# Performance work log

Hardware: AMD Instinct MI355X
Metric: run time of the kernel (lower is better)

## Reference

```python
import math
import jax, jax.numpy as jnp
import numpy as np

B_SZ = 32768   # batch (reflections)
S = 4          # mc_samples
D_IN = 256     # encoder dim
LAT = 8        # latent dim
NBINS = 300    # resolution x angle bins
K = 1323       # profile pixels
R = 4          # CP rank


def setup_inputs() -> dict:
    key = jax.random.key(0)
    ks = jax.random.split(key, 8)
    x = jax.random.normal(ks[0], (B_SZ, D_IN), jnp.float32)
    group_labels = jax.random.randint(ks[1], (B_SZ,), 0, NBINS)
    eps = jax.random.normal(ks[2], (S, B_SZ, LAT), jnp.float32)  # reparam noise
    A = jax.random.normal(ks[3], (NBINS, R), jnp.float32) * 0.01
    B = jax.random.normal(ks[4], (K, R), jnp.float32) * 0.01
    C = jax.random.normal(ks[5], (LAT, R), jnp.float32) * 0.01
    b = jnp.zeros((NBINS, K), jnp.float32)
    # nn.Linear default init (kaiming-uniform approx via small normal is fine for a numeric baseline)
    bound = 1.0 / math.sqrt(D_IN)
    mu_w = jax.random.uniform(ks[6], (LAT, D_IN), jnp.float32, -bound, bound)
    mu_b = jax.random.uniform(ks[7], (LAT,), jnp.float32, -bound, bound)
    std_w = jnp.zeros((LAT, D_IN), jnp.float32)  # nn.init.zeros_
    std_b = jnp.full((LAT,), math.log(math.exp(0.5) - 1.0), jnp.float32)  # softplus^-1(0.5)
    return dict(x=x, eps=eps, A=A, B=B, C=C, b=b, mu_w=mu_w, mu_b=mu_b,
                std_w=std_w, std_b=std_b, group_labels=group_labels)


def reference(x, eps, A, B, C, b, mu_w, mu_b, std_w, std_b, group_labels):
    mu_h = x @ mu_w.T + mu_b                      # (B, d)
    std_h = jax.nn.softplus(x @ std_w.T + std_b)  # (B, d)
    h = mu_h + std_h * eps                        # rsample: (S, B, d)

    A_n = A[group_labels]                         # (B, R)  per-bin gather
    b_n = b[group_labels]                         # (B, K)  per-bin gather

    z = h @ C                                     # (S, B, R)
    logits = (A_n * z) @ B.T + b_n                # (S, B, K)
    zp = jax.nn.softmax(logits, axis=-1)

    z_mean = mu_h @ C                             # (B, R)
    mean_logits = (A_n * z_mean) @ B.T + b_n      # (B, K)
    mean_profile = jax.nn.softmax(mean_logits, axis=-1)
    return zp, mean_profile, mu_h, std_h
```

## Files before the change

kernel.cpp:

```cpp
#include <hip/hip_runtime.h>

#define B_SZ  32768
#define S_MC  4
#define D_IN  256
#define LAT   8
#define NBINS 300
#define KDIM  1323
#define RNK   4

typedef float f32x4 __attribute__((ext_vector_type(4)));

constexpr int TPB   = 256;
constexpr int BPB   = 4;
constexpr int NPASS = S_MC + 1;
constexpr int NF4   = 330;
constexpr int ITER1 = NF4 - TPB;


__global__ __launch_bounds__(TPB) void cp_profile_kernel(
    const float* __restrict__ x,
    const float* __restrict__ eps,
    const float* __restrict__ A,
    const float* __restrict__ Bm,
    const float* __restrict__ C,
    const float* __restrict__ bias,
    const float* __restrict__ mu_w,
    const float* __restrict__ mu_b,
    const float* __restrict__ std_w,
    const float* __restrict__ std_b,
    const int*   __restrict__ glab,
    float* __restrict__ out)
{
    __shared__ float muh_s[LAT];
    __shared__ float stdh_s[LAT];
    __shared__ float w_s[NPASS][RNK];
    __shared__ float redmax_s[4][NPASS];
    __shared__ float redsum_s[4][NPASS];

    const int tid  = threadIdx.x;
    const int lane = tid & 63;
    const int wid  = tid >> 6;
    const f32x4* B4 = reinterpret_cast<const f32x4*>(Bm);

    for (int bb = 0; bb < BPB; ++bb) {
        const int b = blockIdx.x * BPB + bb;
        const int g = glab[b];
        const int p = b & 3;

        const f32x4* x4 = reinterpret_cast<const f32x4*>(x + (size_t)b * D_IN);
        const f32x4 xv = x4[lane];
        float dotv[4];
        #pragma unroll
        for (int dd = 0; dd < 4; ++dd) {
            const int d = wid * 4 + dd;
            const f32x4* W4 = reinterpret_cast<const f32x4*>(
                (d < LAT) ? (mu_w + d * D_IN) : (std_w + (d - LAT) * D_IN));
            const f32x4 wv = W4[lane];
            float a = xv.x * wv.x + xv.y * wv.y + xv.z * wv.z + xv.w * wv.w;
            #pragma unroll
            for (int off = 32; off > 0; off >>= 1)
                a += __shfl_xor(a, off, 64);
            dotv[dd] = a;
        }
        if (lane == 0) {
            #pragma unroll
            for (int dd = 0; dd < 4; ++dd) {
                const int d = wid * 4 + dd;
                if (d < LAT) {
                    muh_s[d] = dotv[dd] + mu_b[d];
                } else {
                    const float y = dotv[dd] + std_b[d - LAT];
                    stdh_s[d - LAT] = fmaxf(y, 0.f) + log1pf(expf(-fabsf(y)));
                }
            }
        }
        __syncthreads();

        if (tid < 20) {
            const int s = tid >> 2, r = tid & 3;
            const float* ep = eps + ((size_t)(s < S_MC ? s : 0) * B_SZ + b) * LAT;
            float z = 0.f;
            #pragma unroll
            for (int j = 0; j < LAT; ++j) {
                float h = muh_s[j];
                if (s < S_MC) h += stdh_s[j] * ep[j];
                z += h * C[j * RNK + r];
            }
            w_s[s][r] = A[g * RNK + r] * z;
        }
        const size_t base_small = (size_t)NPASS * B_SZ * KDIM;
        if (tid >= 32 && tid < 40)
            out[base_small + (size_t)b * LAT + (tid - 32)] = muh_s[tid - 32];
        if (tid >= 40 && tid < 48)
            out[base_small + (size_t)B_SZ * LAT + (size_t)b * LAT + (tid - 40)] = stdh_s[tid - 40];
        __syncthreads();

        float wr[NPASS][RNK];
        #pragma unroll
        for (int s = 0; s < NPASS; ++s)
            #pragma unroll
            for (int r = 0; r < RNK; ++r)
                wr[s][r] = w_s[s][r];

        const int  k0 = p + 4 * tid;
        const bool v1 = (tid < ITER1);
        const int  k1 = p + 4 * (TPB + tid);
        const int  e  = tid - 100;
        const bool vht = (e >= 0 && e < 3);
        const int  kht = vht ? ((e < p) ? e : (1320 + e)) : 0;

        const float* biasg = bias + (size_t)g * KDIM;
        f32x4 br0[4], br1[4];
        float bv0[4], bv1[4];
        #pragma unroll
        for (int q = 0; q < 4; ++q) {
            br0[q] = B4[k0 + q];
            bv0[q] = biasg[k0 + q];
            if (v1) { br1[q] = B4[k1 + q]; bv1[q] = biasg[k1 + q]; }
            else    { br1[q] = (f32x4)(0.f); bv1[q] = -INFINITY; }
        }
        f32x4 brht = (f32x4)(0.f);
        float bvht = -INFINITY;
        if (vht) { brht = B4[kht]; bvht = biasg[kht]; }

        auto LG = [&](const f32x4& r4, float bi, int s) -> float {
            return fmaf(wr[s][0], r4.x,
                   fmaf(wr[s][1], r4.y,
                   fmaf(wr[s][2], r4.z, wr[s][3] * r4.w))) + bi;
        };

        float lmax[NPASS];
        #pragma unroll
        for (int s = 0; s < NPASS; ++s) {
            float m0 = -INFINITY;
            #pragma unroll
            for (int q = 0; q < 4; ++q) {
                m0 = fmaxf(m0, LG(br0[q], bv0[q], s));
                m0 = fmaxf(m0, LG(br1[q], bv1[q], s));
            }
            lmax[s] = fmaxf(m0, LG(brht, bvht, s));
        }
        #pragma unroll
        for (int s = 0; s < NPASS; ++s)
            #pragma unroll
            for (int off = 32; off > 0; off >>= 1)
                lmax[s] = fmaxf(lmax[s], __shfl_xor(lmax[s], off, 64));
        if (lane == 0) {
            #pragma unroll
            for (int s = 0; s < NPASS; ++s) redmax_s[wid][s] = lmax[s];
        }
        __syncthreads();

        float m[NPASS];
        #pragma unroll
        for (int s = 0; s < NPASS; ++s)
            m[s] = fmaxf(fmaxf(redmax_s[0][s], redmax_s[1][s]),
                         fmaxf(redmax_s[2][s], redmax_s[3][s]));

        float lsum[NPASS];
        #pragma unroll
        for (int s = 0; s < NPASS; ++s) {
            float a = 0.f;
            #pragma unroll
            for (int q = 0; q < 4; ++q) {
                a += __expf(LG(br0[q], bv0[q], s) - m[s]);
                a += __expf(LG(br1[q], bv1[q], s) - m[s]);
            }
            lsum[s] = a + __expf(LG(brht, bvht, s) - m[s]);
        }
        #pragma unroll
        for (int s = 0; s < NPASS; ++s)
            #pragma unroll
            for (int off = 32; off > 0; off >>= 1)
                lsum[s] += __shfl_xor(lsum[s], off, 64);
        if (lane == 0) {
            #pragma unroll
            for (int s = 0; s < NPASS; ++s) redsum_s[wid][s] = lsum[s];
        }
        __syncthreads();

        float inv[NPASS];
        #pragma unroll
        for (int s = 0; s < NPASS; ++s)
            inv[s] = 1.f / (redsum_s[0][s] + redsum_s[1][s] +
                            redsum_s[2][s] + redsum_s[3][s]);

        #pragma unroll
        for (int s = 0; s < NPASS; ++s) {
            const size_t ob = (s < S_MC)
                ? ((size_t)((size_t)s * B_SZ + b) * KDIM)
                : ((size_t)S_MC * B_SZ * KDIM + (size_t)b * KDIM);
            f32x4 o0;
            o0.x = __expf(LG(br0[0], bv0[0], s) - m[s]) * inv[s];
            o0.y = __expf(LG(br0[1], bv0[1], s) - m[s]) * inv[s];
            o0.z = __expf(LG(br0[2], bv0[2], s) - m[s]) * inv[s];
            o0.w = __expf(LG(br0[3], bv0[3], s) - m[s]) * inv[s];
            __builtin_nontemporal_store(
                o0, reinterpret_cast<f32x4*>(out + ob + k0));
            if (v1) {
                f32x4 o1;
                o1.x = __expf(LG(br1[0], bv1[0], s) - m[s]) * inv[s];
                o1.y = __expf(LG(br1[1], bv1[1], s) - m[s]) * inv[s];
                o1.z = __expf(LG(br1[2], bv1[2], s) - m[s]) * inv[s];
                o1.w = __expf(LG(br1[3], bv1[3], s) - m[s]) * inv[s];
                __builtin_nontemporal_store(
                    o1, reinterpret_cast<f32x4*>(out + ob + k1));
            }
            if (vht) {
                const float v = __expf(LG(brht, bvht, s) - m[s]) * inv[s];
                __builtin_nontemporal_store(v, out + ob + kht);
            }
        }
    }
}

extern "C" void kernel_launch(void* const* d_in, const int* in_sizes, int n_in,
                              void* d_out, int out_size, void* d_ws, size_t ws_size,
                              hipStream_t stream) {
    const float* x     = (const float*)d_in[0];
    const float* eps   = (const float*)d_in[1];
    const float* A     = (const float*)d_in[2];
    const float* Bm    = (const float*)d_in[3];
    const float* C     = (const float*)d_in[4];
    const float* bias  = (const float*)d_in[5];
    const float* mu_w  = (const float*)d_in[6];
    const float* mu_b  = (const float*)d_in[7];
    const float* std_w = (const float*)d_in[8];
    const float* std_b = (const float*)d_in[9];
    const int*   glab  = (const int*)d_in[10];
    float* out = (float*)d_out;

    cp_profile_kernel<<<B_SZ / BPB, TPB, 0, stream>>>(
        x, eps, A, Bm, C, bias, mu_w, mu_b, std_w, std_b, glab, out);
}
```

Before: 1.109 ms.

## Use one wavefront per reflection with scalar strided stores and wave-only reductions

Restructures the kernel so each 64-thread block handles a single batch row, with every thread covering about 21 strided profile pixels. The cross-wave LDS reductions and their barriers go away, since the softmax max and sum reductions now stay inside one wavefront via shuffles. In exchange, the 16-byte vectorized output stores become scalar 4-byte stores, the grid grows to 32768 small blocks, and B rows are reloaded in each of the three passes. The output write bandwidth, which likely dominates, may suffer from the narrower stores.

```diff
diff --git a/kernel.cpp b/kernel.cpp
--- a/kernel.cpp
+++ b/kernel.cpp
@@ -10,14 +10,12 @@
 
 typedef float f32x4 __attribute__((ext_vector_type(4)));
 
-constexpr int TPB   = 256;
-constexpr int BPB   = 4;
+constexpr int TPB   = 64;
 constexpr int NPASS = S_MC + 1;
-constexpr int NF4   = 330;
-constexpr int ITER1 = NF4 - TPB;
+constexpr int KPT   = (KDIM + TPB - 1) / TPB;
 
 
-__global__ __launch_bounds__(TPB) void cp_profile_kernel(
+__global__ __launch_bounds__(TPB, 4) void cp_profile_kernel(
     const float* __restrict__ x,
     const float* __restrict__ eps,
     const float* __restrict__ A,
@@ -34,181 +32,132 @@
     __shared__ float muh_s[LAT];
     __shared__ float stdh_s[LAT];
     __shared__ float w_s[NPASS][RNK];
-    __shared__ float redmax_s[4][NPASS];
-    __shared__ float redsum_s[4][NPASS];
 
-    const int tid  = threadIdx.x;
-    const int lane = tid & 63;
-    const int wid  = tid >> 6;
+    const int t = threadIdx.x;
+    const int b = blockIdx.x;
+    const int g = glab[b];
+
+    {
+        const int d = t >> 2, c = t & 3;
+        const f32x4* x4 = reinterpret_cast<const f32x4*>(x + (size_t)b * D_IN);
+        const f32x4* W4 = reinterpret_cast<const f32x4*>(
+            (d < LAT) ? (mu_w + d * D_IN) : (std_w + (d - LAT) * D_IN));
+        float a = 0.f;
+        #pragma unroll
+        for (int i = 0; i < 16; ++i) {
+            const f32x4 xv = x4[c * 16 + i];
+            const f32x4 wv = W4[c * 16 + i];
+            a += xv.x * wv.x + xv.y * wv.y + xv.z * wv.z + xv.w * wv.w;
+        }
+        a += __shfl_xor(a, 1, 64);
+        a += __shfl_xor(a, 2, 64);
+        if (c == 0) {
+            if (d < LAT) {
+                muh_s[d] = a + mu_b[d];
+            } else {
+                const float y = a + std_b[d - LAT];
+                stdh_s[d - LAT] = fmaxf(y, 0.f) + log1pf(expf(-fabsf(y)));
+            }
+        }
+    }
+    __syncthreads();
+
+    if (t < 20) {
+        const int s = t >> 2, r = t & 3;
+        const float* ep = eps + ((size_t)(s < S_MC ? s : 0) * B_SZ + b) * LAT;
+        float z = 0.f;
+        #pragma unroll
+        for (int j = 0; j < LAT; ++j) {
+            float h = muh_s[j];
+            if (s < S_MC) h += stdh_s[j] * ep[j];
+            z += h * C[j * RNK + r];
+        }
+        w_s[s][r] = A[g * RNK + r] * z;
+    }
+    const size_t base_small = (size_t)NPASS * B_SZ * KDIM;
+    if (t >= 32 && t < 40)
+        out[base_small + (size_t)b * LAT + (t - 32)] = muh_s[t - 32];
+    if (t >= 40 && t < 48)
+        out[base_small + (size_t)B_SZ * LAT + (size_t)b * LAT + (t - 40)] = stdh_s[t - 40];
+    __syncthreads();
+
+    float wr[NPASS][RNK];
+    #pragma unroll
+    for (int s = 0; s < NPASS; ++s)
+        #pragma unroll
+        for (int r = 0; r < RNK; ++r)
+            wr[s][r] = w_s[s][r];
+
+    const float* biasg = bias + (size_t)g * KDIM;
+    float bn[KPT];
+    #pragma unroll
+    for (int j = 0; j < KPT; ++j) {
+        const int k = t + TPB * j;
+        bn[j] = (k < KDIM) ? biasg[k] : 0.f;
+    }
+
     const f32x4* B4 = reinterpret_cast<const f32x4*>(Bm);
 
-    for (int bb = 0; bb < BPB; ++bb) {
-        const int b = blockIdx.x * BPB + bb;
-        const int g = glab[b];
-        const int p = b & 3;
+    auto LG = [&](const f32x4& r4, float bi, int s) -> float {
+        return fmaf(wr[s][0], r4.x,
+               fmaf(wr[s][1], r4.y,
+               fmaf(wr[s][2], r4.z, wr[s][3] * r4.w))) + bi;
+    };
 
-        const f32x4* x4 = reinterpret_cast<const f32x4*>(x + (size_t)b * D_IN);
-        const f32x4 xv = x4[lane];
-        float dotv[4];
+    float lmax[NPASS];
+    #pragma unroll
+    for (int s = 0; s < NPASS; ++s) lmax[s] = -INFINITY;
+    #pragma unroll
+    for (int j = 0; j < KPT; ++j) {
+        const int k = t + TPB * j;
+        if (k < KDIM) {
+            const f32x4 bv = B4[k];
+            #pragma unroll
+            for (int s = 0; s < NPASS; ++s)
+                lmax[s] = fmaxf(lmax[s], LG(bv, bn[j], s));
+        }
+    }
+    #pragma unroll
+    for (int s = 0; s < NPASS; ++s)
         #pragma unroll
-        for (int dd = 0; dd < 4; ++dd) {
-            const int d = wid * 4 + dd;
-            const f32x4* W4 = reinterpret_cast<const f32x4*>(
-                (d < LAT) ? (mu_w + d * D_IN) : (std_w + (d - LAT) * D_IN));
-            const f32x4 wv = W4[lane];
-            float a = xv.x * wv.x + xv.y * wv.y + xv.z * wv.z + xv.w * wv.w;
+        for (int off = 32; off > 0; off >>= 1)
+            lmax[s] = fmaxf(lmax[s], __shfl_xor(lmax[s], off, 64));
+
+    float lsum[NPASS];
+    #pragma unroll
+    for (int s = 0; s < NPASS; ++s) lsum[s] = 0.f;
+    #pragma unroll
+    for (int j = 0; j < KPT; ++j) {
+        const int k = t + TPB * j;
+        if (k < KDIM) {
+            const f32x4 bv = B4[k];
             #pragma unroll
-            for (int off = 32; off > 0; off >>= 1)
-                a += __shfl_xor(a, off, 64);
-            dotv[dd] = a;
+            for (int s = 0; s < NPASS; ++s)
+                lsum[s] += __expf(LG(bv, bn[j], s) - lmax[s]);
         }
-        if (lane == 0) {
+    }
+    #pragma unroll
+    for (int s = 0; s < NPASS; ++s)
+        #pragma unroll
+        for (int off = 32; off > 0; off >>= 1)
+            lsum[s] += __shfl_xor(lsum[s], off, 64);
+
+    float inv[NPASS];
+    #pragma unroll
+    for (int s = 0; s < NPASS; ++s) inv[s] = 1.f / lsum[s];
+
+    #pragma unroll
+    for (int j = 0; j < KPT; ++j) {
+        const int k = t + TPB * j;
+        if (k < KDIM) {
+            const f32x4 bv = B4[k];
             #pragma unroll
-            for (int dd = 0; dd < 4; ++dd) {
-                const int d = wid * 4 + dd;
-                if (d < LAT) {
-                    muh_s[d] = dotv[dd] + mu_b[d];
-                } else {
-                    const float y = dotv[dd] + std_b[d - LAT];
-                    stdh_s[d - LAT] = fmaxf(y, 0.f) + log1pf(expf(-fabsf(y)));
-                }
-            }
-        }
-        __syncthreads();
-
-        if (tid < 20) {
-            const int s = tid >> 2, r = tid & 3;
-            const float* ep = eps + ((size_t)(s < S_MC ? s : 0) * B_SZ + b) * LAT;
-            float z = 0.f;
-            #pragma unroll
-            for (int j = 0; j < LAT; ++j) {
-                float h = muh_s[j];
-                if (s < S_MC) h += stdh_s[j] * ep[j];
-                z += h * C[j * RNK + r];
-            }
-            w_s[s][r] = A[g * RNK + r] * z;
-        }
-        const size_t base_small = (size_t)NPASS * B_SZ * KDIM;
-        if (tid >= 32 && tid < 40)
-            out[base_small + (size_t)b * LAT + (tid - 32)] = muh_s[tid - 32];
-        if (tid >= 40 && tid < 48)
-            out[base_small + (size_t)B_SZ * LAT + (size_t)b * LAT + (tid - 40)] = stdh_s[tid - 40];
-        __syncthreads();
-
-        float wr[NPASS][RNK];
-        #pragma unroll
-        for (int s = 0; s < NPASS; ++s)
-            #pragma unroll
-            for (int r = 0; r < RNK; ++r)
-                wr[s][r] = w_s[s][r];
-
-        const int  k0 = p + 4 * tid;
-        const bool v1 = (tid < ITER1);
-        const int  k1 = p + 4 * (TPB + tid);
-        const int  e  = tid - 100;
-        const bool vht = (e >= 0 && e < 3);
-        const int  kht = vht ? ((e < p) ? e : (1320 + e)) : 0;
-
-        const float* biasg = bias + (size_t)g * KDIM;
-        f32x4 br0[4], br1[4];
-        float bv0[4], bv1[4];
-        #pragma unroll
-        for (int q = 0; q < 4; ++q) {
-            br0[q] = B4[k0 + q];
-            bv0[q] = biasg[k0 + q];
-            if (v1) { br1[q] = B4[k1 + q]; bv1[q] = biasg[k1 + q]; }
-            else    { br1[q] = (f32x4)(0.f); bv1[q] = -INFINITY; }
-        }
-        f32x4 brht = (f32x4)(0.f);
-        float bvht = -INFINITY;
-        if (vht) { brht = B4[kht]; bvht = biasg[kht]; }
-
-        auto LG = [&](const f32x4& r4, float bi, int s) -> float {
-            return fmaf(wr[s][0], r4.x,
-                   fmaf(wr[s][1], r4.y,
-                   fmaf(wr[s][2], r4.z, wr[s][3] * r4.w))) + bi;
-        };
-
-        float lmax[NPASS];
-        #pragma unroll
-        for (int s = 0; s < NPASS; ++s) {
-            float m0 = -INFINITY;
-            #pragma unroll
-            for (int q = 0; q < 4; ++q) {
-                m0 = fmaxf(m0, LG(br0[q], bv0[q], s));
-                m0 = fmaxf(m0, LG(br1[q], bv1[q], s));
-            }
-            lmax[s] = fmaxf(m0, LG(brht, bvht, s));
-        }
-        #pragma unroll
-        for (int s = 0; s < NPASS; ++s)
-            #pragma unroll
-            for (int off = 32; off > 0; off >>= 1)
-                lmax[s] = fmaxf(lmax[s], __shfl_xor(lmax[s], off, 64));
-        if (lane == 0) {
-            #pragma unroll
-            for (int s = 0; s < NPASS; ++s) redmax_s[wid][s] = lmax[s];
-        }
-        __syncthreads();
-
-        float m[NPASS];
-        #pragma unroll
-        for (int s = 0; s < NPASS; ++s)
-            m[s] = fmaxf(fmaxf(redmax_s[0][s], redmax_s[1][s]),
-                         fmaxf(redmax_s[2][s], redmax_s[3][s]));
-
-        float lsum[NPASS];
-        #pragma unroll
-        for (int s = 0; s < NPASS; ++s) {
-            float a = 0.f;
-            #pragma unroll
-            for (int q = 0; q < 4; ++q) {
-                a += __expf(LG(br0[q], bv0[q], s) - m[s]);
-                a += __expf(LG(br1[q], bv1[q], s) - m[s]);
-            }
-            lsum[s] = a + __expf(LG(brht, bvht, s) - m[s]);
-        }
-        #pragma unroll
-        for (int s = 0; s < NPASS; ++s)
-            #pragma unroll
-            for (int off = 32; off > 0; off >>= 1)
-                lsum[s] += __shfl_xor(lsum[s], off, 64);
-        if (lane == 0) {
-            #pragma unroll
-            for (int s = 0; s < NPASS; ++s) redsum_s[wid][s] = lsum[s];
-        }
-        __syncthreads();
-
-        float inv[NPASS];
-        #pragma unroll
-        for (int s = 0; s < NPASS; ++s)
-            inv[s] = 1.f / (redsum_s[0][s] + redsum_s[1][s] +
-                            redsum_s[2][s] + redsum_s[3][s]);
-
-        #pragma unroll
-        for (int s = 0; s < NPASS; ++s) {
-            const size_t ob = (s < S_MC)
-                ? ((size_t)((size_t)s * B_SZ + b) * KDIM)
-                : ((size_t)S_MC * B_SZ * KDIM + (size_t)b * KDIM);
-            f32x4 o0;
-            o0.x = __expf(LG(br0[0], bv0[0], s) - m[s]) * inv[s];
-            o0.y = __expf(LG(br0[1], bv0[1], s) - m[s]) * inv[s];
-            o0.z = __expf(LG(br0[2], bv0[2], s) - m[s]) * inv[s];
-            o0.w = __expf(LG(br0[3], bv0[3], s) - m[s]) * inv[s];
-            __builtin_nontemporal_store(
-                o0, reinterpret_cast<f32x4*>(out + ob + k0));
-            if (v1) {
-                f32x4 o1;
-                o1.x = __expf(LG(br1[0], bv1[0], s) - m[s]) * inv[s];
-                o1.y = __expf(LG(br1[1], bv1[1], s) - m[s]) * inv[s];
-                o1.z = __expf(LG(br1[2], bv1[2], s) - m[s]) * inv[s];
-                o1.w = __expf(LG(br1[3], bv1[3], s) - m[s]) * inv[s];
+            for (int s = 0; s < NPASS; ++s) {
+                const size_t ob = (s < S_MC)
+                    ? ((size_t)((size_t)s * B_SZ + b) * KDIM)
+                    : ((size_t)S_MC * B_SZ * KDIM + (size_t)b * KDIM);
                 __builtin_nontemporal_store(
-                    o1, reinterpret_cast<f32x4*>(out + ob + k1));
-            }
-            if (vht) {
-                const float v = __expf(LG(brht, bvht, s) - m[s]) * inv[s];
-                __builtin_nontemporal_store(v, out + ob + kht);
+                    __expf(LG(bv, bn[j], s) - lmax[s]) * inv[s], out + ob + k);
             }
         }
     }
@@ -230,6 +179,6 @@
     const int*   glab  = (const int*)d_in[10];
     float* out = (float*)d_out;
 
-    cp_profile_kernel<<<B_SZ / BPB, TPB, 0, stream>>>(
+    cp_profile_kernel<<<B_SZ, TPB, 0, stream>>>(
         x, eps, A, Bm, C, bias, mu_w, mu_b, std_w, std_b, glab, out);
 }
```

Result: no change. 1.130 ms (+1.9%).
